# Kernel optimization log

Hardware: AMD Instinct MI355X
Metric: run time of the kernel (lower is better)

## Reference

```python
import jax, jax.numpy as jnp
import numpy as np

N_NODES = 100000
N_EDGES = 3200000
F = 32          # n_node_features
L = 50          # n_node_labels
EL = 10         # n_edge_labels
K = 16          # out_dim (graph_data.num_classes)


def setup_inputs() -> dict:
    key = jax.random.key(0)
    ks = jax.random.split(key, 12)
    x = jax.random.normal(ks[0], (N_NODES, F), dtype=jnp.float32)
    node_labels = jax.random.randint(ks[1], (N_NODES,), 0, L, dtype=jnp.int32)
    edge_src = jax.random.randint(ks[2], (N_EDGES,), 0, N_NODES, dtype=jnp.int32)
    edge_dst = jax.random.randint(ks[3], (N_EDGES,), 0, N_NODES, dtype=jnp.int32)
    edge_labels = jax.random.randint(ks[4], (N_EDGES,), 0, EL, dtype=jnp.int32)
    s = 0.1
    W1 = jax.random.normal(ks[5], (L, L, EL), dtype=jnp.float32) * s
    b1 = jax.random.normal(ks[6], (L,), dtype=jnp.float32) * s
    W2 = jax.random.normal(ks[7], (L, L, EL), dtype=jnp.float32) * s
    b2 = jax.random.normal(ks[8], (L,), dtype=jnp.float32) * s
    W3 = jax.random.normal(ks[9], (L, L, EL), dtype=jnp.float32) * s
    b3 = jax.random.normal(ks[10], (L,), dtype=jnp.float32) * s
    kr1, kr2 = jax.random.split(ks[11])
    Wr = jax.random.normal(kr1, (L, F, K), dtype=jnp.float32) * s
    br = jax.random.normal(kr2, (K,), dtype=jnp.float32) * s
    return {"x": x, "W1": W1, "b1": b1, "W2": W2, "b2": b2, "W3": W3, "b3": b3,
            "Wr": Wr, "br": br, "node_labels": node_labels,
            "edge_src": edge_src, "edge_dst": edge_dst, "edge_labels": edge_labels}


def _conv(x, W, b, node_labels, edge_src, edge_dst, edge_labels):
    # weight_rule_wf: per-edge scalar weight indexed by (src label, dst label, edge label)
    w_e = W[node_labels[edge_src], node_labels[edge_dst], edge_labels]  # [E]
    msgs = w_e[:, None] * x[edge_src]                                   # [E, F]
    agg = jax.ops.segment_sum(msgs, edge_dst, num_segments=x.shape[0])  # [N, F]
    # node_label_rule bias: per-node bias indexed by node label, then Tanh
    return jnp.tanh(agg + b[node_labels][:, None])


def reference(x, W1, b1, W2, b2, W3, b3, Wr, br,
              node_labels, edge_src, edge_dst, edge_labels):
    h = _conv(x, W1, b1, node_labels, edge_src, edge_dst, edge_labels)
    h = _conv(h, W2, b2, node_labels, edge_src, edge_dst, edge_labels)
    h = _conv(h, W3, b3, node_labels, edge_src, edge_dst, edge_labels)
    # GraphResizeLayer (node_label_rule): out[k] = sum_i Wr[label_i, f, k] * h[i, f] + br[k]
    # equivalent efficient form: pre-aggregate node features by label, then contract.
    sums = jax.ops.segment_sum(h, node_labels, num_segments=Wr.shape[0])  # [L, F]
    out = jnp.tanh(jnp.einsum('lf,lfk->k', sums, Wr) + br)                # [K]
    return out
```

## Files before the change

kernel.cpp:

```cpp
#include <hip/hip_runtime.h>
#include <hip/hip_bf16.h>
#include <hip/hip_fp8.h>

#define NN 100000
#define NE 3200000
#define FF 32
#define LL 50
#define ELB 10
#define KK 16

#define CH 8192
#define NBLK_P1 391
#define NBUK 391
#define CAP 9216

typedef float floatx2 __attribute__((ext_vector_type(2)));

__device__ __forceinline__ float fast_tanh(float x) {
    float e = __expf(2.0f * x);
    return 1.0f - 2.0f / (e + 1.0f);
}

__global__ __launch_bounds__(512) void p1_scatter(const int* __restrict__ esrc,
                                                  const int* __restrict__ edst,
                                                  const int* __restrict__ elab,
                                                  const float* __restrict__ x,
                                                  unsigned* __restrict__ xb,
                                                  int* __restrict__ cursor,
                                                  unsigned* __restrict__ recs) {
    __shared__ int lcnt[NBUK];
    __shared__ int lbase[NBUK];
    __shared__ int sdst[CH];
    int tid = threadIdx.x;
    for (int i = blockIdx.x * 512 + tid; i < NN * FF / 4; i += NBLK_P1 * 512) {
        float4 v = ((const float4*)x)[i];
        __hip_fp8_e4m3 a(v.x), b(v.y), c(v.z), d(v.w);
        xb[i] = (unsigned)a.__x | ((unsigned)b.__x << 8) |
                ((unsigned)c.__x << 16) | ((unsigned)d.__x << 24);
    }
    for (int i = tid; i < NBUK; i += 512) lcnt[i] = 0;
    __syncthreads();
    long e0 = (long)blockIdx.x * CH;
    long rem = NE - e0;
    int cnt = rem < CH ? (int)rem : CH;
    int nq = cnt >> 2;
    const int4* edst4 = (const int4*)(edst + e0);
    const int4* esrc4 = (const int4*)(esrc + e0);
    const int4* elab4 = (const int4*)(elab + e0);
    for (int i = tid; i < nq; i += 512) {
        int4 d = edst4[i];
        ((int4*)sdst)[i] = d;
        atomicAdd(&lcnt[d.x >> 8], 1);
        atomicAdd(&lcnt[d.y >> 8], 1);
        atomicAdd(&lcnt[d.z >> 8], 1);
        atomicAdd(&lcnt[d.w >> 8], 1);
    }
    __syncthreads();
    for (int i = tid; i < NBUK; i += 512) {
        int c = lcnt[i];
        lbase[i] = c ? atomicAdd(&cursor[i], c) : 0;
        lcnt[i] = 0;
    }
    __syncthreads();
    for (int i = tid; i < nq; i += 512) {
        int4 s4 = esrc4[i];
        int4 l4 = elab4[i];
        int4 d4 = ((const int4*)sdst)[i];
#pragma unroll
        for (int k = 0; k < 4; ++k) {
            int s  = (&s4.x)[k];
            int d  = (&d4.x)[k];
            int el = (&l4.x)[k];
            int b = d >> 8;
            int ofs = atomicAdd(&lcnt[b], 1);
            int rel = lbase[b] + ofs;
            if (rel < CAP)
                recs[b * CAP + rel] =
                    ((unsigned)s << 12) | ((unsigned)el << 8) | (unsigned)(d & 255);
        }
    }
}

__global__ __launch_bounds__(256) void p2_local(const int* __restrict__ cursor,
                                                const unsigned* __restrict__ recs,
                                                const int* __restrict__ labels,
                                                unsigned* __restrict__ packed,
                                                int* __restrict__ gstart,
                                                int* __restrict__ gcnt) {
    __shared__ int deg[256], loff[256], lcur[256], sc[256], labd[256];
    int b = blockIdx.x, tid = threadIdx.x;
    int base = b * CAP;
    int n = cursor[b];
    if (n > CAP) n = CAP;
    int node = (b << 8) + tid;
    deg[tid] = 0;
    lcur[tid] = 0;
    labd[tid] = (node < NN) ? labels[node] : 0;
    __syncthreads();
    for (int i = tid; i < n; i += 256)
        atomicAdd(&deg[(int)(recs[base + i] & 255)], 1);
    __syncthreads();
    sc[tid] = deg[tid];
    __syncthreads();
    for (int ofs = 1; ofs < 256; ofs <<= 1) {
        int t = (tid >= ofs) ? sc[tid - ofs] : 0;
        __syncthreads();
        sc[tid] += t;
        __syncthreads();
    }
    loff[tid] = sc[tid] - deg[tid];
    if (node < NN) { gstart[node] = base + loff[tid]; gcnt[node] = deg[tid]; }
    __syncthreads();
    for (int i = tid; i < n; i += 256) {
        unsigned r = recs[base + i];
        int dl  = (int)(r & 255);
        int el  = (int)((r >> 8) & 15);
        int src = (int)(r >> 12);
        int widx = labels[src] * (LL * ELB) + labd[dl] * ELB + el;
        int ofs = atomicAdd(&lcur[dl], 1);
        packed[base + loff[dl] + ofs] = ((unsigned)widx << 17) | (unsigned)src;
    }
}

__global__ __launch_bounds__(256) void conv_kernel(const unsigned char* __restrict__ xin,
                                                   unsigned char* __restrict__ hout,
                                                   const int* __restrict__ gstart,
                                                   const int* __restrict__ gcnt,
                                                   const unsigned* __restrict__ packed,
                                                   const float* __restrict__ Wtab,
                                                   const float* __restrict__ bias,
                                                   const int* __restrict__ labels) {
    __shared__ unsigned stage[8][64];
    int tid = threadIdx.x;
    int hw = tid >> 5, lane = tid & 31;
    int node = (blockIdx.x << 3) + hw;
    int s = gstart[node];
    int n = gcnt[node];
    int eg = lane >> 3;
    int fg = (lane & 7) << 2;
    float4 acc = {0.f, 0.f, 0.f, 0.f};
    for (int base = 0; base < n; base += 32) {
        float w = 0.f;
        unsigned so = 0u;
        int idx = base + lane;
        if (idx < n) {
            unsigned p = packed[s + idx];
            w = Wtab[p >> 17];
            so = (p & 0x1FFFFu) << 5;
        }
        ((uint2*)&stage[hw][0])[lane] = make_uint2(__float_as_uint(w), so);
        __builtin_amdgcn_wave_barrier();
#pragma unroll
        for (int j = 0; j < 8; ++j) {
            uint2 ws = ((const uint2*)&stage[hw][0])[j * 4 + eg];
            unsigned pv = *(const unsigned*)(xin + ws.y + fg);
            floatx2 lo = __builtin_amdgcn_cvt_pk_f32_fp8((int)pv, false);
            floatx2 hi = __builtin_amdgcn_cvt_pk_f32_fp8((int)pv, true);
            float we = __uint_as_float(ws.x);
            acc.x += we * lo.x;
            acc.y += we * lo.y;
            acc.z += we * hi.x;
            acc.w += we * hi.y;
        }
        __builtin_amdgcn_wave_barrier();
    }
    acc.x += __shfl_xor(acc.x, 8);  acc.y += __shfl_xor(acc.y, 8);
    acc.z += __shfl_xor(acc.z, 8);  acc.w += __shfl_xor(acc.w, 8);
    acc.x += __shfl_xor(acc.x, 16); acc.y += __shfl_xor(acc.y, 16);
    acc.z += __shfl_xor(acc.z, 16); acc.w += __shfl_xor(acc.w, 16);
    if (lane < 8) {
        float bb = bias[labels[node]];
        __hip_fp8_e4m3 q0(fast_tanh(acc.x + bb));
        __hip_fp8_e4m3 q1(fast_tanh(acc.y + bb));
        __hip_fp8_e4m3 q2(fast_tanh(acc.z + bb));
        __hip_fp8_e4m3 q3(fast_tanh(acc.w + bb));
        unsigned pk = (unsigned)q0.__x | ((unsigned)q1.__x << 8) |
                      ((unsigned)q2.__x << 16) | ((unsigned)q3.__x << 24);
        ((unsigned*)(hout + ((long)node << 5)))[lane] = pk;
    }
}

__global__ __launch_bounds__(256) void lsum_kernel(const unsigned* __restrict__ h,
                                                   const int* __restrict__ labels,
                                                   float* __restrict__ sums) {
    __shared__ float ls[LL * FF];
    int tid = threadIdx.x;
    for (int i = tid; i < LL * FF; i += 256) ls[i] = 0.f;
    __syncthreads();
    for (int i = blockIdx.x * 256 + tid; i < NN * 8; i += gridDim.x * 256) {
        unsigned pv = h[i];
        int nodei = i >> 3;
        int fb = (i & 7) << 2;
        int l = labels[nodei];
        floatx2 lo = __builtin_amdgcn_cvt_pk_f32_fp8((int)pv, false);
        floatx2 hi = __builtin_amdgcn_cvt_pk_f32_fp8((int)pv, true);
        float* bp = &ls[l * FF + fb];
        atomicAdd(bp + 0, lo.x);
        atomicAdd(bp + 1, lo.y);
        atomicAdd(bp + 2, hi.x);
        atomicAdd(bp + 3, hi.y);
    }
    __syncthreads();
    for (int i = tid; i < LL * FF; i += 256) atomicAdd(&sums[i], ls[i]);
}

__global__ __launch_bounds__(256) void resize_kernel(const float* __restrict__ sums,
                                                     const float* __restrict__ Wr,
                                                     const float* __restrict__ br,
                                                     float* __restrict__ out) {
    __shared__ float red[256][KK];
    int tid = threadIdx.x;
    float acc[KK];
#pragma unroll
    for (int k = 0; k < KK; ++k) acc[k] = 0.f;
    for (int p = tid; p < LL * FF; p += 256) {
        float sv = sums[p];
#pragma unroll
        for (int k = 0; k < KK; ++k) acc[k] += sv * Wr[p * KK + k];
    }
#pragma unroll
    for (int k = 0; k < KK; ++k) red[tid][k] = acc[k];
    __syncthreads();
    for (int sft = 128; sft > 0; sft >>= 1) {
        if (tid < sft) {
#pragma unroll
            for (int k = 0; k < KK; ++k) red[tid][k] += red[tid + sft][k];
        }
        __syncthreads();
    }
    if (tid < KK) out[tid] = fast_tanh(red[0][tid] + br[tid]);
}

extern "C" void kernel_launch(void* const* d_in, const int* in_sizes, int n_in,
                              void* d_out, int out_size, void* d_ws, size_t ws_size,
                              hipStream_t stream) {
    const float* x   = (const float*)d_in[0];
    const float* W1  = (const float*)d_in[1];
    const float* b1  = (const float*)d_in[2];
    const float* W2  = (const float*)d_in[3];
    const float* b2  = (const float*)d_in[4];
    const float* W3  = (const float*)d_in[5];
    const float* b3  = (const float*)d_in[6];
    const float* Wr  = (const float*)d_in[7];
    const float* br  = (const float*)d_in[8];
    const int* labels = (const int*)d_in[9];
    const int* esrc   = (const int*)d_in[10];
    const int* edst   = (const int*)d_in[11];
    const int* elab   = (const int*)d_in[12];
    float* out = (float*)d_out;

    char* ws = (char*)d_ws;
    size_t o = 0;
    auto alloc = [&](size_t bytes) -> void* {
        void* p = ws + o;
        o += (bytes + 255) & ~(size_t)255;
        return p;
    };
    char* regionA = (char*)alloc((size_t)NBUK * CAP * sizeof(unsigned));
    unsigned* recs = (unsigned*)regionA;
    unsigned char* h1 = (unsigned char*)regionA;
    unsigned char* h2 = (unsigned char*)(regionA + (size_t)NN * FF);

    unsigned* packed = (unsigned*)alloc((size_t)NBUK * CAP * sizeof(unsigned));
    unsigned* xb     = (unsigned*)alloc((size_t)NN * FF);
    int* cursor = (int*)alloc(NBUK * sizeof(int));
    float* sums = (float*)alloc(LL * FF * sizeof(float));
    int* gstart = (int*)alloc(NN * sizeof(int));
    int* gcnt   = (int*)alloc(NN * sizeof(int));

    size_t msz = (size_t)((char*)sums - (char*)cursor) + LL * FF * sizeof(float);
    hipMemsetAsync(cursor, 0, msz, stream);

    p1_scatter<<<NBLK_P1, 512, 0, stream>>>(esrc, edst, elab, x, xb, cursor, recs);
    p2_local<<<NBUK, 256, 0, stream>>>(cursor, recs, labels, packed, gstart, gcnt);

    conv_kernel<<<NN / 8, 256, 0, stream>>>((const unsigned char*)xb, h1, gstart, gcnt, packed, W1, b1, labels);
    conv_kernel<<<NN / 8, 256, 0, stream>>>(h1, h2, gstart, gcnt, packed, W2, b2, labels);
    conv_kernel<<<NN / 8, 256, 0, stream>>>(h2, h1, gstart, gcnt, packed, W3, b3, labels);

    lsum_kernel<<<128, 256, 0, stream>>>((const unsigned*)h1, labels, sums);
    resize_kernel<<<1, 256, 0, stream>>>(sums, Wr, br, out);
}
```

Before: 318.1 us.

## Widen dst buckets to 512 nodes, drop LDS staging in conv gather loop

Destination buckets now span 512 nodes instead of 256, which halves the bucket count and doubles per-bucket capacity, and the local sort kernel now runs with 512 threads. The scatter kernel no longer caches dst indices in shared memory and rereads them from global memory instead. The conv kernel drops the shared-memory staging of weights and offsets: each lane group reads packed records directly with a 4-way unrolled loop, giving more independent loads in flight and removing the wave barriers. In exchange, lanes issue redundant packed and weight loads, and the record encoding moves src up to bit 13, so src must still fit in the remaining bits.

```diff
diff --git a/kernel.cpp b/kernel.cpp
--- a/kernel.cpp
+++ b/kernel.cpp
@@ -11,8 +11,8 @@
 
 #define CH 8192
 #define NBLK_P1 391
-#define NBUK 391
-#define CAP 9216
+#define NBUK 196
+#define CAP 18432
 
 typedef float floatx2 __attribute__((ext_vector_type(2)));
 
@@ -30,7 +30,6 @@
                                                   unsigned* __restrict__ recs) {
     __shared__ int lcnt[NBUK];
     __shared__ int lbase[NBUK];
-    __shared__ int sdst[CH];
     int tid = threadIdx.x;
     for (int i = blockIdx.x * 512 + tid; i < NN * FF / 4; i += NBLK_P1 * 512) {
         float4 v = ((const float4*)x)[i];
@@ -49,11 +48,10 @@
     const int4* elab4 = (const int4*)(elab + e0);
     for (int i = tid; i < nq; i += 512) {
         int4 d = edst4[i];
-        ((int4*)sdst)[i] = d;
-        atomicAdd(&lcnt[d.x >> 8], 1);
-        atomicAdd(&lcnt[d.y >> 8], 1);
-        atomicAdd(&lcnt[d.z >> 8], 1);
-        atomicAdd(&lcnt[d.w >> 8], 1);
+        atomicAdd(&lcnt[d.x >> 9], 1);
+        atomicAdd(&lcnt[d.y >> 9], 1);
+        atomicAdd(&lcnt[d.z >> 9], 1);
+        atomicAdd(&lcnt[d.w >> 9], 1);
     }
     __syncthreads();
     for (int i = tid; i < NBUK; i += 512) {
@@ -65,44 +63,44 @@
     for (int i = tid; i < nq; i += 512) {
         int4 s4 = esrc4[i];
         int4 l4 = elab4[i];
-        int4 d4 = ((const int4*)sdst)[i];
+        int4 d4 = edst4[i];
 #pragma unroll
         for (int k = 0; k < 4; ++k) {
             int s  = (&s4.x)[k];
             int d  = (&d4.x)[k];
             int el = (&l4.x)[k];
-            int b = d >> 8;
+            int b = d >> 9;
             int ofs = atomicAdd(&lcnt[b], 1);
             int rel = lbase[b] + ofs;
             if (rel < CAP)
                 recs[b * CAP + rel] =
-                    ((unsigned)s << 12) | ((unsigned)el << 8) | (unsigned)(d & 255);
+                    ((unsigned)s << 13) | ((unsigned)el << 9) | (unsigned)(d & 511);
         }
     }
 }
 
-__global__ __launch_bounds__(256) void p2_local(const int* __restrict__ cursor,
+__global__ __launch_bounds__(512) void p2_local(const int* __restrict__ cursor,
                                                 const unsigned* __restrict__ recs,
                                                 const int* __restrict__ labels,
                                                 unsigned* __restrict__ packed,
                                                 int* __restrict__ gstart,
                                                 int* __restrict__ gcnt) {
-    __shared__ int deg[256], loff[256], lcur[256], sc[256], labd[256];
+    __shared__ int deg[512], loff[512], lcur[512], sc[512], labd[512];
     int b = blockIdx.x, tid = threadIdx.x;
     int base = b * CAP;
     int n = cursor[b];
     if (n > CAP) n = CAP;
-    int node = (b << 8) + tid;
+    int node = (b << 9) + tid;
     deg[tid] = 0;
     lcur[tid] = 0;
     labd[tid] = (node < NN) ? labels[node] : 0;
     __syncthreads();
-    for (int i = tid; i < n; i += 256)
-        atomicAdd(&deg[(int)(recs[base + i] & 255)], 1);
+    for (int i = tid; i < n; i += 512)
+        atomicAdd(&deg[(int)(recs[base + i] & 511)], 1);
     __syncthreads();
     sc[tid] = deg[tid];
     __syncthreads();
-    for (int ofs = 1; ofs < 256; ofs <<= 1) {
+    for (int ofs = 1; ofs < 512; ofs <<= 1) {
         int t = (tid >= ofs) ? sc[tid - ofs] : 0;
         __syncthreads();
         sc[tid] += t;
@@ -111,11 +109,11 @@
     loff[tid] = sc[tid] - deg[tid];
     if (node < NN) { gstart[node] = base + loff[tid]; gcnt[node] = deg[tid]; }
     __syncthreads();
-    for (int i = tid; i < n; i += 256) {
+    for (int i = tid; i < n; i += 512) {
         unsigned r = recs[base + i];
-        int dl  = (int)(r & 255);
-        int el  = (int)((r >> 8) & 15);
-        int src = (int)(r >> 12);
+        int dl  = (int)(r & 511);
+        int el  = (int)((r >> 9) & 15);
+        int src = (int)(r >> 13);
         int widx = labels[src] * (LL * ELB) + labd[dl] * ELB + el;
         int ofs = atomicAdd(&lcur[dl], 1);
         packed[base + loff[dl] + ofs] = ((unsigned)widx << 17) | (unsigned)src;
@@ -130,39 +128,46 @@
                                                    const float* __restrict__ Wtab,
                                                    const float* __restrict__ bias,
                                                    const int* __restrict__ labels) {
-    __shared__ unsigned stage[8][64];
     int tid = threadIdx.x;
     int hw = tid >> 5, lane = tid & 31;
     int node = (blockIdx.x << 3) + hw;
-    int s = gstart[node];
-    int n = gcnt[node];
     int eg = lane >> 3;
     int fg = (lane & 7) << 2;
+    int i   = gstart[node] + eg;
+    int end = gstart[node] + gcnt[node];
     float4 acc = {0.f, 0.f, 0.f, 0.f};
-    for (int base = 0; base < n; base += 32) {
-        float w = 0.f;
-        unsigned so = 0u;
-        int idx = base + lane;
-        if (idx < n) {
-            unsigned p = packed[s + idx];
-            w = Wtab[p >> 17];
-            so = (p & 0x1FFFFu) << 5;
-        }
-        ((uint2*)&stage[hw][0])[lane] = make_uint2(__float_as_uint(w), so);
-        __builtin_amdgcn_wave_barrier();
-#pragma unroll
-        for (int j = 0; j < 8; ++j) {
-            uint2 ws = ((const uint2*)&stage[hw][0])[j * 4 + eg];
-            unsigned pv = *(const unsigned*)(xin + ws.y + fg);
-            floatx2 lo = __builtin_amdgcn_cvt_pk_f32_fp8((int)pv, false);
-            floatx2 hi = __builtin_amdgcn_cvt_pk_f32_fp8((int)pv, true);
-            float we = __uint_as_float(ws.x);
-            acc.x += we * lo.x;
-            acc.y += we * lo.y;
-            acc.z += we * hi.x;
-            acc.w += we * hi.y;
-        }
-        __builtin_amdgcn_wave_barrier();
+    for (; i + 12 < end; i += 16) {
+        unsigned p0 = packed[i];
+        unsigned p1 = packed[i + 4];
+        unsigned p2 = packed[i + 8];
+        unsigned p3 = packed[i + 12];
+        float w0 = Wtab[p0 >> 17], w1 = Wtab[p1 >> 17];
+        float w2 = Wtab[p2 >> 17], w3 = Wtab[p3 >> 17];
+        unsigned v0 = *(const unsigned*)(xin + ((p0 & 0x1FFFFu) << 5) + fg);
+        unsigned v1 = *(const unsigned*)(xin + ((p1 & 0x1FFFFu) << 5) + fg);
+        unsigned v2 = *(const unsigned*)(xin + ((p2 & 0x1FFFFu) << 5) + fg);
+        unsigned v3 = *(const unsigned*)(xin + ((p3 & 0x1FFFFu) << 5) + fg);
+        floatx2 lo, hi;
+        lo = __builtin_amdgcn_cvt_pk_f32_fp8((int)v0, false);
+        hi = __builtin_amdgcn_cvt_pk_f32_fp8((int)v0, true);
+        acc.x += w0 * lo.x; acc.y += w0 * lo.y; acc.z += w0 * hi.x; acc.w += w0 * hi.y;
+        lo = __builtin_amdgcn_cvt_pk_f32_fp8((int)v1, false);
+        hi = __builtin_amdgcn_cvt_pk_f32_fp8((int)v1, true);
+        acc.x += w1 * lo.x; acc.y += w1 * lo.y; acc.z += w1 * hi.x; acc.w += w1 * hi.y;
+        lo = __builtin_amdgcn_cvt_pk_f32_fp8((int)v2, false);
+        hi = __builtin_amdgcn_cvt_pk_f32_fp8((int)v2, true);
+        acc.x += w2 * lo.x; acc.y += w2 * lo.y; acc.z += w2 * hi.x; acc.w += w2 * hi.y;
+        lo = __builtin_amdgcn_cvt_pk_f32_fp8((int)v3, false);
+        hi = __builtin_amdgcn_cvt_pk_f32_fp8((int)v3, true);
+        acc.x += w3 * lo.x; acc.y += w3 * lo.y; acc.z += w3 * hi.x; acc.w += w3 * hi.y;
+    }
+    for (; i < end; i += 4) {
+        unsigned p = packed[i];
+        float w = Wtab[p >> 17];
+        unsigned v = *(const unsigned*)(xin + ((p & 0x1FFFFu) << 5) + fg);
+        floatx2 lo = __builtin_amdgcn_cvt_pk_f32_fp8((int)v, false);
+        floatx2 hi = __builtin_amdgcn_cvt_pk_f32_fp8((int)v, true);
+        acc.x += w * lo.x; acc.y += w * lo.y; acc.z += w * hi.x; acc.w += w * hi.y;
     }
     acc.x += __shfl_xor(acc.x, 8);  acc.y += __shfl_xor(acc.y, 8);
     acc.z += __shfl_xor(acc.z, 8);  acc.w += __shfl_xor(acc.w, 8);
@@ -272,7 +277,7 @@
     hipMemsetAsync(cursor, 0, msz, stream);
 
     p1_scatter<<<NBLK_P1, 512, 0, stream>>>(esrc, edst, elab, x, xb, cursor, recs);
-    p2_local<<<NBUK, 256, 0, stream>>>(cursor, recs, labels, packed, gstart, gcnt);
+    p2_local<<<NBUK, 512, 0, stream>>>(cursor, recs, labels, packed, gstart, gcnt);
 
     conv_kernel<<<NN / 8, 256, 0, stream>>>((const unsigned char*)xb, h1, gstart, gcnt, packed, W1, b1, labels);
     conv_kernel<<<NN / 8, 256, 0, stream>>>(h1, h2, gstart, gcnt, packed, W2, b2, labels);
```

Result: slower. 328.0 us (+3.1%).
